# Kernel optimization log

Hardware: AMD Instinct MI355X
Metric: run time of the kernel (lower is better)

Reference implementation:

```python
import jax, jax.numpy as jnp
import numpy as np

D_MODEL = 1024
HEADS = 16
HEAD_DIM = D_MODEL // HEADS


def setup_inputs() -> dict:
    key = jax.random.key(0)
    k1, k2 = jax.random.split(key)
    x = jax.random.normal(k1, (2, 2048, D_MODEL), dtype=jnp.float32)
    # nn.Linear(d_model, 3*d_model, bias=False): weight shape [3*d_model, d_model]
    W_qkv = jax.random.normal(k2, (3 * D_MODEL, D_MODEL), dtype=jnp.float32) * (D_MODEL ** -0.5)
    return {"x": x, "W_qkv": W_qkv}


def reference(x, W_qkv):
    b, t, c = x.shape
    qkv = jnp.einsum('btc,fc->btf', x, W_qkv)  # [b, t, 3c]
    q, k, v = jnp.split(qkv, 3, axis=-1)
    # [b, heads, t, head_dim]
    q = q.reshape(b, t, HEADS, HEAD_DIM).transpose(0, 2, 1, 3)
    k = k.reshape(b, t, HEADS, HEAD_DIM).transpose(0, 2, 1, 3)
    v = v.reshape(b, t, HEADS, HEAD_DIM).transpose(0, 2, 1, 3)
    scores = jnp.einsum('bhqd,bhkd->bhqk', q, k) * (HEAD_DIM ** -0.5)
    causal = jnp.tril(jnp.ones((t, t), dtype=bool))  # [t, t]
    scores = jnp.where(causal[None, None, :, :], scores, -jnp.inf)
    weights = jax.nn.softmax(scores, axis=-1)
    out = jnp.einsum('bhqk,bhkd->bhqd', weights, v)
    return out.transpose(0, 2, 1, 3).reshape(b, t, c)
```

## Files before the change

kernel.cpp:

```cpp
#include <hip/hip_runtime.h>
#include <hip/hip_bf16.h>
#include <stdint.h>

#define D_MODEL 1024
#define TOKENS  2048
#define HEADS   16
#define HDIM    64
#define NQKV    3072
#define MROWS   4096
#define SCALE   0.18033688011112042f

typedef __attribute__((ext_vector_type(4)))  float f32x4;
typedef __attribute__((ext_vector_type(16))) float f32x16;
typedef __attribute__((ext_vector_type(8)))  short bf16x8;

__device__ __forceinline__ unsigned short f2bf(float f) {
  union { float f; unsigned u; } v; v.f = f;
  unsigned u = v.u + 0x7FFFu + ((v.u >> 16) & 1u);
  return (unsigned short)(u >> 16);
}
__device__ __forceinline__ float bf2f(unsigned short b) {
  union { unsigned u; float f; } v; v.u = ((unsigned)b) << 16;
  return v.f;
}
__device__ __forceinline__ unsigned cvt_pk_bf16(float lo, float hi) {
  unsigned r;
  asm("v_cvt_pk_bf16_f32 %0, %1, %2" : "=v"(r) : "v"(lo), "v"(hi));
  return r;
}
__device__ __forceinline__ float xchg32(float v) {
  return __shfl_xor(v, 32);
}
__device__ __forceinline__ bf16x8 pfrag8(const float* g) {
  union { uint4 u; bf16x8 v; } r;
  r.u.x = cvt_pk_bf16(g[0], g[1]);
  r.u.y = cvt_pk_bf16(g[2], g[3]);
  r.u.z = cvt_pk_bf16(g[4], g[5]);
  r.u.w = cvt_pk_bf16(g[6], g[7]);
  return r.v;
}
__device__ __forceinline__ float max32t(const f32x16& a, const f32x16& b) {
  float t[16];
#pragma unroll
  for (int r = 0; r < 16; ++r) t[r] = fmaxf(a[r], b[r]);
#pragma unroll
  for (int s = 8; s > 0; s >>= 1)
#pragma unroll
    for (int r = 0; r < s; ++r) t[r] = fmaxf(t[r], t[r + s]);
  return t[0];
}
__device__ __forceinline__ float sum32t(const float* a, const float* b) {
  float t[16];
#pragma unroll
  for (int r = 0; r < 16; ++r) t[r] = a[r] + b[r];
#pragma unroll
  for (int s = 8; s > 0; s >>= 1)
#pragma unroll
    for (int r = 0; r < s; ++r) t[r] = t[r] + t[r + s];
  return t[0];
}

#define GLOAD16(g, l)                                                          \
  __builtin_amdgcn_global_load_lds(                                            \
      (const __attribute__((address_space(1))) unsigned int*)(g),              \
      (__attribute__((address_space(3))) unsigned int*)(l), 16, 0, 0)

__global__ __launch_bounds__(256) void cvt_bf16(const float* __restrict__ X,
                                                const float* __restrict__ W,
                                                unsigned short* __restrict__ Xb,
                                                unsigned short* __restrict__ Wb) {
  const size_t NX = (size_t)MROWS * D_MODEL;
  size_t i = ((size_t)blockIdx.x * 256 + threadIdx.x) * 8;
  const float* src; unsigned short* dst; size_t off;
  if (i < NX) { src = X; dst = Xb; off = i; }
  else        { src = W; dst = Wb; off = i - NX; }
  float4 a = ((const float4*)(src + off))[0];
  float4 b = ((const float4*)(src + off))[1];
  union { unsigned short s[8]; uint4 v; } u;
  u.s[0] = f2bf(a.x); u.s[1] = f2bf(a.y); u.s[2] = f2bf(a.z); u.s[3] = f2bf(a.w);
  u.s[4] = f2bf(b.x); u.s[5] = f2bf(b.y); u.s[6] = f2bf(b.z); u.s[7] = f2bf(b.w);
  *(uint4*)(dst + off) = u.v;
}

__global__ __launch_bounds__(512, 1) void gemm8(const unsigned short* __restrict__ A,
                                                const unsigned short* __restrict__ B,
                                                unsigned short* __restrict__ C) {
  __shared__ unsigned short sA[2][2][128][64];
  __shared__ unsigned short sB[2][2][128][64];

  const int tid  = threadIdx.x;
  const int lane = tid & 63;
  const int wave = tid >> 6;
  const int wr   = wave >> 2;
  const int wc   = wave & 3;
  const int l15  = lane & 15;
  const int lg   = lane >> 4;

  const int bm = blockIdx.x;
  const int bn = blockIdx.y;

  f32x4 acc[8][4];
#pragma unroll
  for (int i = 0; i < 8; ++i)
#pragma unroll
    for (int j = 0; j < 4; ++j)
#pragma unroll
      for (int r = 0; r < 4; ++r) acc[i][j][r] = 0.f;

  const int srow = tid >> 3;
  const int scb  = (tid & 7) * 16;
  const int ssce = (scb ^ ((srow & 7) << 4)) >> 1;

  const unsigned short* Ag = A + (size_t)(bm * 256) * D_MODEL;
  const unsigned short* Bg = B + (size_t)(bn * 256) * D_MODEL;

#define STG_A(buf, hf, t)                                                      \
  { GLOAD16(Ag + (size_t)((hf) * 128 + srow) * D_MODEL + (t) * 64 + ssce,      \
            (char*)&sA[buf][hf][0][0] + srow * 128 + scb);                     \
    GLOAD16(Ag + (size_t)((hf) * 128 + 64 + srow) * D_MODEL + (t) * 64 + ssce, \
            (char*)&sA[buf][hf][0][0] + 8192 + srow * 128 + scb); }
#define STG_B(buf, hf, t)                                                      \
  { GLOAD16(Bg + (size_t)((hf) * 128 + srow) * D_MODEL + (t) * 64 + ssce,      \
            (char*)&sB[buf][hf][0][0] + srow * 128 + scb);                     \
    GLOAD16(Bg + (size_t)((hf) * 128 + 64 + srow) * D_MODEL + (t) * 64 + ssce, \
            (char*)&sB[buf][hf][0][0] + 8192 + srow * 128 + scb); }

  const char* aBse[2] = { (const char*)&sA[0][wr][0][0], (const char*)&sA[1][wr][0][0] };
  const char* bBse[2] = { (const char*)&sB[0][wc >> 1][0][0], (const char*)&sB[1][wc >> 1][0][0] };
  const int swzl = (l15 & 7) << 4;
  const int cbs0 = (lg * 16) ^ swzl;
  const int cbs1 = (64 + lg * 16) ^ swzl;
  const int arow = l15 * 128;
  const int brow = ((wc & 1) * 64 + l15) * 128;

  bf16x8 aF[4][2];

#define DO_PHASE(qm, qn, buf, LD_A, STAGE_STMT, DO_VM)                         \
  {                                                                            \
    if (LD_A) {                                                                \
      _Pragma("unroll")                                                        \
      for (int i = 0; i < 4; ++i) {                                            \
        aF[i][0] = *(const bf16x8*)(aBse[buf] + ((qm)*4 + i) * 2048 + arow + cbs0); \
        aF[i][1] = *(const bf16x8*)(aBse[buf] + ((qm)*4 + i) * 2048 + arow + cbs1); \
      }                                                                        \
    }                                                                          \
    bf16x8 b_[2][2];                                                           \
    _Pragma("unroll")                                                          \
    for (int n = 0; n < 2; ++n) {                                              \
      b_[n][0] = *(const bf16x8*)(bBse[buf] + ((qn)*2 + n) * 2048 + brow + cbs0); \
      b_[n][1] = *(const bf16x8*)(bBse[buf] + ((qn)*2 + n) * 2048 + brow + cbs1); \
    }                                                                          \
    STAGE_STMT;                                                                \
    if (DO_VM) asm volatile("s_waitcnt vmcnt(2)" ::: "memory");                \
    __builtin_amdgcn_s_barrier();                                              \
    asm volatile("s_waitcnt lgkmcnt(0)" ::: "memory");                         \
    __builtin_amdgcn_sched_barrier(0);                                         \
    __builtin_amdgcn_s_setprio(1);                                             \
    _Pragma("unroll")                                                          \
    for (int ks = 0; ks < 2; ++ks)                                             \
      _Pragma("unroll")                                                        \
      for (int i = 0; i < 4; ++i)                                              \
        _Pragma("unroll")                                                      \
        for (int n = 0; n < 2; ++n)                                            \
          acc[(qm)*4 + i][(qn)*2 + n] = __builtin_amdgcn_mfma_f32_16x16x32_bf16( \
              aF[i][ks], b_[n][ks], acc[(qm)*4 + i][(qn)*2 + n], 0, 0, 0);     \
    __builtin_amdgcn_s_setprio(0);                                             \
    __builtin_amdgcn_s_barrier();                                              \
  }

  STG_A(0, 0, 0);
  STG_B(0, 0, 0);
  STG_A(0, 1, 0);
  STG_B(0, 1, 0);
  STG_B(1, 0, 1);
  asm volatile("s_waitcnt vmcnt(2)" ::: "memory");
  __builtin_amdgcn_s_barrier();

#pragma unroll 1
  for (int j = 0; j < 8; ++j) {
    const int t1 = 2 * j + 1;
    const int t2 = 2 * j + 2;
    const int t3 = 2 * j + 3;
    DO_PHASE(0, 0, 0, 1, { STG_A(1, 0, t1); }, 0);
    DO_PHASE(0, 1, 0, 0, { STG_A(1, 1, t1); }, 0);
    DO_PHASE(1, 0, 0, 1, { STG_B(1, 1, t1); }, 0);
    DO_PHASE(1, 1, 0, 0, { if (t2 < 16) STG_B(0, 0, t2); }, 1);
    DO_PHASE(0, 0, 1, 1, { if (t2 < 16) STG_A(0, 0, t2); }, 0);
    DO_PHASE(0, 1, 1, 0, { if (t2 < 16) STG_A(0, 1, t2); }, 0);
    DO_PHASE(1, 0, 1, 1, { if (t2 < 16) STG_B(0, 1, t2); }, 0);
    DO_PHASE(1, 1, 1, 0, { if (t3 < 16) STG_B(1, 0, t3); }, 1);
  }

  const int orow0 = bm * 256 + wr * 128 + lg * 4;
  const int ocol0 = bn * 256 + wc * 64 + l15;
#pragma unroll
  for (int mi = 0; mi < 8; ++mi)
#pragma unroll
    for (int ni = 0; ni < 4; ++ni)
#pragma unroll
      for (int r = 0; r < 4; ++r)
        C[(size_t)(orow0 + mi * 16 + r) * NQKV + ocol0 + ni * 16] = f2bf(acc[mi][ni][r]);
#undef STG_A
#undef STG_B
#undef DO_PHASE
}

__global__ __launch_bounds__(256) void qkv_gemm(const float* __restrict__ X,
                                                const float* __restrict__ W,
                                                unsigned short* __restrict__ QKV) {
  __shared__ unsigned short sA[128 * 32];
  __shared__ unsigned short sB[128 * 32];
  const int tid  = threadIdx.x;
  const int lane = tid & 63;
  const int wave = tid >> 6;
  const int wr = wave >> 1, wc = wave & 1;
  const int row0 = blockIdx.x * 128;
  const int col0 = blockIdx.y * 128;

  f32x4 acc[4][4];
#pragma unroll
  for (int i = 0; i < 4; ++i)
#pragma unroll
    for (int j = 0; j < 4; ++j)
#pragma unroll
      for (int r = 0; r < 4; ++r) acc[i][j][r] = 0.f;

  const int srow = tid >> 1;
  const int scol = (tid & 1) * 16;
  union U16 { unsigned short s[8]; uint4 v; };

#pragma unroll 1
  for (int k0 = 0; k0 < D_MODEL; k0 += 32) {
    {
      const float* ga = X + (size_t)(row0 + srow) * D_MODEL + k0 + scol;
      const float* gb = W + (size_t)(col0 + srow) * D_MODEL + k0 + scol;
      float va[16], vb[16];
#pragma unroll
      for (int i = 0; i < 4; ++i) {
        float4 t = ((const float4*)ga)[i];
        va[4*i+0] = t.x; va[4*i+1] = t.y; va[4*i+2] = t.z; va[4*i+3] = t.w;
        float4 u = ((const float4*)gb)[i];
        vb[4*i+0] = u.x; vb[4*i+1] = u.y; vb[4*i+2] = u.z; vb[4*i+3] = u.w;
      }
      U16 ua0, ua1, ub0, ub1;
#pragma unroll
      for (int e = 0; e < 8; ++e) {
        ua0.s[e] = f2bf(va[e]);   ua1.s[e] = f2bf(va[8 + e]);
        ub0.s[e] = f2bf(vb[e]);   ub1.s[e] = f2bf(vb[8 + e]);
      }
      *(uint4*)&sA[srow * 32 + scol + 0] = ua0.v;
      *(uint4*)&sA[srow * 32 + scol + 8] = ua1.v;
      *(uint4*)&sB[srow * 32 + scol + 0] = ub0.v;
      *(uint4*)&sB[srow * 32 + scol + 8] = ub1.v;
    }
    __syncthreads();

    const int lrow = lane & 15;
    const int lk   = (lane >> 4) * 8;
    bf16x8 av[4], bv[4];
#pragma unroll
    for (int i = 0; i < 4; ++i)
      av[i] = *(const bf16x8*)&sA[(wr * 64 + i * 16 + lrow) * 32 + lk];
#pragma unroll
    for (int j = 0; j < 4; ++j)
      bv[j] = *(const bf16x8*)&sB[(wc * 64 + j * 16 + lrow) * 32 + lk];
#pragma unroll
    for (int i = 0; i < 4; ++i)
#pragma unroll
      for (int j = 0; j < 4; ++j)
        acc[i][j] = __builtin_amdgcn_mfma_f32_16x16x32_bf16(av[i], bv[j], acc[i][j], 0, 0, 0);
    __syncthreads();
  }

  const int orow = row0 + wr * 64 + (lane >> 4) * 4;
  const int ocol = col0 + wc * 64 + (lane & 15);
#pragma unroll
  for (int i = 0; i < 4; ++i)
#pragma unroll
    for (int j = 0; j < 4; ++j)
#pragma unroll
      for (int r = 0; r < 4; ++r)
        QKV[(size_t)(orow + i * 16 + r) * NQKV + ocol + j * 16] = f2bf(acc[i][j][r]);
}

__global__ __launch_bounds__(256, 2) void attn12(const unsigned short* __restrict__ QKV,
                                                 float* __restrict__ Out) {
  __shared__ unsigned short sK [2][2][64 * 64];
  __shared__ unsigned short sVt[2][2][64 * 64];

  const int tid  = threadIdx.x;
  const int lane = tid & 63;
  const int wave = tid >> 6;
  const int l31  = lane & 31;
  const int hi   = lane >> 5;

  const int x = blockIdx.x;
  int bh, u;
  if (x < 256) { bh = x & 31; u = x >> 5; }
  else         { const int x2 = x - 256; bh = x2 & 31; u = 15 - (x2 >> 5); }

  const int b = bh >> 4, h = bh & 15;
  const int q0w  = u * 128 + wave * 32;
  const int qcol = q0w + l31;

  const unsigned short* Qbase = QKV + (size_t)(b * TOKENS) * NQKV + h * HDIM;
  const unsigned short* Kbase = Qbase + D_MODEL;
  const unsigned short* Vbase = Kbase + D_MODEL;

  bf16x8 qf[4];
  {
    const unsigned short* qrow = Qbase + (size_t)qcol * NQKV + hi * 8;
    union { unsigned short us[8]; bf16x8 v; ushort4 q[2]; } t;
#pragma unroll
    for (int dk = 0; dk < 4; ++dk) {
      t.q[0] = ((const ushort4*)(qrow + dk * 16))[0];
      t.q[1] = ((const ushort4*)(qrow + dk * 16))[1];
#pragma unroll
      for (int e = 0; e < 8; ++e) t.us[e] = f2bf(bf2f(t.us[e]) * SCALE);
      qf[dk] = t.v;
    }
  }

  f32x16 o0a, o0b, o1a, o1b;
#pragma unroll
  for (int r = 0; r < 16; ++r) { o0a[r] = 0.f; o0b[r] = 0.f; o1a[r] = 0.f; o1b[r] = 0.f; }
  float m = -1e30f, ll = 0.f;

  const int vk0 = (tid & 15) * 4;
  const int vd0 = (tid >> 4) * 4;
  ushort4 va0, va1, va2, va3, vb0, vb1, vb2, vb3;

  const int lane16 = lane * 16;

#define KGLOAD(kt, buf, s)                                                     \
  {                                                                            \
    _Pragma("unroll")                                                          \
    for (int g = 0; g < 2; ++g) {                                              \
      const int base = g * 4096 + wave * 1024;                                 \
      const int d = base + lane16;                                             \
      const int row = d >> 7;                                                  \
      const int grow = (row & 51) | ((row & 4) << 1) | ((row & 8) >> 1);       \
      const int cb = (d & 127) ^ ((row & 7) << 4);                             \
      GLOAD16(Kbase + (size_t)((kt) * 64 + grow) * NQKV + (cb >> 1),           \
              (char*)&sK[buf][s][0] + base + lane16);                          \
    }                                                                          \
  }

#define VLOAD2(pp)                                                             \
  {                                                                            \
    const unsigned short* vsA = Vbase + (size_t)((2*(pp)) * 64 + vk0) * NQKV + vd0;   \
    va0 = *(const ushort4*)(vsA);                                              \
    va1 = *(const ushort4*)(vsA + NQKV);                                       \
    va2 = *(const ushort4*)(vsA + 2 * NQKV);                                   \
    va3 = *(const ushort4*)(vsA + 3 * NQKV);                                   \
    const unsigned short* vsB = Vbase + (size_t)((2*(pp)+1) * 64 + vk0) * NQKV + vd0; \
    vb0 = *(const ushort4*)(vsB);                                              \
    vb1 = *(const ushort4*)(vsB + NQKV);                                       \
    vb2 = *(const ushort4*)(vsB + 2 * NQKV);                                   \
    vb3 = *(const ushort4*)(vsB + 3 * NQKV);                                   \
  }

#define VWRITE1(buf, s, t0, t1, t2, t3)                                        \
  {                                                                            \
    ushort4 c0, c1, c2, c3;                                                    \
    c0.x = t0.x; c0.y = t1.x; c0.z = t2.x; c0.w = t3.x;                        \
    c1.x = t0.y; c1.y = t1.y; c1.z = t2.y; c1.w = t3.y;                        \
    c2.x = t0.z; c2.y = t1.z; c2.z = t2.z; c2.w = t3.z;                        \
    c3.x = t0.w; c3.y = t1.w; c3.z = t2.w; c3.w = t3.w;                        \
    char* dV = (char*)&sVt[buf][s][0];                                         \
    _Pragma("unroll")                                                          \
    for (int e = 0; e < 4; ++e) {                                              \
      const int dim = vd0 + e;                                                 \
      const int o2 = (dim * 128 + vk0 * 2) ^ ((dim & 7) << 4);                 \
      ushort4 cc = (e == 0) ? c0 : (e == 1) ? c1 : (e == 2) ? c2 : c3;         \
      *(ushort4*)(dV + o2) = cc;                                               \
    }                                                                          \
  }

#define QKT(cK, rowbase, st)                                                   \
  {                                                                            \
    _Pragma("unroll")                                                          \
    for (int dk = 0; dk < 4; ++dk) {                                           \
      const int row = (rowbase);                                               \
      bf16x8 kf = *(const bf16x8*)((cK) + ((row * 128 + hi * 16 + dk * 32) ^ ((row & 7) << 4))); \
      st = __builtin_amdgcn_mfma_f32_32x32x16_bf16(kf, qf[dk], st, 0, 0, 0);   \
    }                                                                          \
  }

#define PV4(cV, bpX, bpY, koff)                                                \
  {                                                                            \
    const int r0 = l31, r1 = l31 + 32;                                         \
    bf16x8 vf;                                                                 \
    vf = *(const bf16x8*)((cV) + ((r0 * 128 + hi * 16 + (koff)) ^ ((r0 & 7) << 4)));      \
    o0a = __builtin_amdgcn_mfma_f32_32x32x16_bf16(vf, bpX, o0a, 0, 0, 0);      \
    vf = *(const bf16x8*)((cV) + ((r1 * 128 + hi * 16 + (koff)) ^ ((r1 & 7) << 4)));      \
    o1a = __builtin_amdgcn_mfma_f32_32x32x16_bf16(vf, bpX, o1a, 0, 0, 0);      \
    vf = *(const bf16x8*)((cV) + ((r0 * 128 + hi * 16 + (koff) + 32) ^ ((r0 & 7) << 4))); \
    o0b = __builtin_amdgcn_mfma_f32_32x32x16_bf16(vf, bpY, o0b, 0, 0, 0);      \
    vf = *(const bf16x8*)((cV) + ((r1 * 128 + hi * 16 + (koff) + 32) ^ ((r1 & 7) << 4))); \
    o1b = __builtin_amdgcn_mfma_f32_32x32x16_bf16(vf, bpY, o1b, 0, 0, 0);      \
  }

#define MUPDATE(mx)                                                            \
  {                                                                            \
    if (!__all((mx) - m <= 8.f)) {                                             \
      float mw = fmaxf((mx), xchg32(mx));                                      \
      const float mnew = fmaxf(m, mw);                                         \
      const float corr = exp2f(m - mnew);                                      \
      m = mnew;                                                                \
      ll *= corr;                                                              \
      _Pragma("unroll")                                                        \
      for (int r = 0; r < 16; ++r) {                                           \
        o0a[r] *= corr; o0b[r] *= corr; o1a[r] *= corr; o1b[r] *= corr;        \
      }                                                                        \
    }                                                                          \
  }

  KGLOAD(0, 0, 0);
  KGLOAD(1, 0, 1);
  VLOAD2(0);
  VWRITE1(0, 0, va0, va1, va2, va3);
  VWRITE1(0, 1, vb0, vb1, vb2, vb3);
  __syncthreads();

#pragma unroll 1
  for (int p = 0; p < u; ++p) {
    const int cur = p & 1;
    KGLOAD(2 * (p + 1),     cur ^ 1, 0);
    KGLOAD(2 * (p + 1) + 1, cur ^ 1, 1);
    VLOAD2(p + 1);

    const char* cKA = (const char*)&sK[cur][0][0];
    const char* cKB = (const char*)&sK[cur][1][0];
    const char* cVA = (const char*)&sVt[cur][0][0];
    const char* cVB = (const char*)&sVt[cur][1][0];

    f32x16 sA0, sA1, sB0, sB1;
#pragma unroll
    for (int r = 0; r < 16; ++r) { sA0[r] = 0.f; sA1[r] = 0.f; sB0[r] = 0.f; sB1[r] = 0.f; }

    QKT(cKA, l31,      sA0);
    QKT(cKA, l31 + 32, sA1);
    QKT(cKB, l31,      sB0);
    QKT(cKB, l31 + 32, sB1);

    {
      float mx = max32t(sA0, sA1);
      MUPDATE(mx);
      float pA0[16], pA1[16];
#pragma unroll
      for (int r = 0; r < 16; ++r) { pA0[r] = exp2f(sA0[r] - m); pA1[r] = exp2f(sA1[r] - m); }
      ll += sum32t(pA0, pA1);
      bf16x8 a0 = pfrag8(&pA0[0]), a1 = pfrag8(&pA0[8]);
      bf16x8 a2 = pfrag8(&pA1[0]), a3 = pfrag8(&pA1[8]);
      PV4(cVA, a0, a1, 0);
      PV4(cVA, a2, a3, 64);
    }

    {
      float mx = max32t(sB0, sB1);
      MUPDATE(mx);
      float pB0[16], pB1[16];
#pragma unroll
      for (int r = 0; r < 16; ++r) { pB0[r] = exp2f(sB0[r] - m); pB1[r] = exp2f(sB1[r] - m); }
      ll += sum32t(pB0, pB1);
      bf16x8 b0 = pfrag8(&pB0[0]), b1 = pfrag8(&pB0[8]);
      bf16x8 b2 = pfrag8(&pB1[0]), b3 = pfrag8(&pB1[8]);
      PV4(cVB, b0, b1, 0);
      PV4(cVB, b2, b3, 64);
    }

    VWRITE1(cur ^ 1, 0, va0, va1, va2, va3);
    VWRITE1(cur ^ 1, 1, vb0, vb1, vb2, vb3);
    __syncthreads();
  }

  {
    const int cur = u & 1;
    const char* cK[2] = { (const char*)&sK[cur][0][0], (const char*)&sK[cur][1][0] };
    const char* cV[2] = { (const char*)&sVt[cur][0][0], (const char*)&sVt[cur][1][0] };
    const int nsub = (wave >= 2) ? 2 : 1;
#pragma unroll 1
    for (int s = 0; s < nsub; ++s) {
      const int kbase = u * 128 + s * 64;
      const bool diag  = (wave >= 2) ? (s == 1) : true;
      const bool do_hi = diag ? ((wave & 1) == 1) : true;

      f32x16 st0, st1;
#pragma unroll
      for (int r = 0; r < 16; ++r) { st0[r] = 0.f; st1[r] = 0.f; }

      QKT(cK[s], l31, st0);
      if (do_hi) QKT(cK[s], l31 + 32, st1);

      if (diag) {
#pragma unroll
        for (int r = 0; r < 16; ++r) {
          const int key0 = kbase + (r & 7) + ((r & 8) << 1) + 8 * hi;
          if (key0 > qcol) st0[r] = -1e30f;
          if (do_hi && key0 + 32 > qcol) st1[r] = -1e30f;
        }
      }

      float mx = do_hi ? max32t(st0, st1) : max32t(st0, st0);
      MUPDATE(mx);

      float p0[16], p1[16];
#pragma unroll
      for (int r = 0; r < 16; ++r) p0[r] = exp2f(st0[r] - m);
      if (do_hi) {
#pragma unroll
        for (int r = 0; r < 16; ++r) p1[r] = exp2f(st1[r] - m);
        ll += sum32t(p0, p1);
      } else {
        float z[16];
#pragma unroll
        for (int r = 0; r < 16; ++r) z[r] = 0.f;
        ll += sum32t(p0, z);
      }

      bf16x8 c0 = pfrag8(&p0[0]), c1 = pfrag8(&p0[8]);
      PV4(cV[s], c0, c1, 0);
      if (do_hi) {
        bf16x8 c2 = pfrag8(&p1[0]), c3 = pfrag8(&p1[8]);
        PV4(cV[s], c2, c3, 64);
      }
    }
  }

  {
    const float lfull = ll + xchg32(ll);
    const float inv = 1.f / lfull;
    float* orow = Out + (size_t)(b * TOKENS + qcol) * D_MODEL + h * HDIM;
#pragma unroll
    for (int g = 0; g < 4; ++g) {
      float4 w0, w1;
      w0.x = (o0a[4*g+0] + o0b[4*g+0]) * inv;
      w0.y = (o0a[4*g+1] + o0b[4*g+1]) * inv;
      w0.z = (o0a[4*g+2] + o0b[4*g+2]) * inv;
      w0.w = (o0a[4*g+3] + o0b[4*g+3]) * inv;
      w1.x = (o1a[4*g+0] + o1b[4*g+0]) * inv;
      w1.y = (o1a[4*g+1] + o1b[4*g+1]) * inv;
      w1.z = (o1a[4*g+2] + o1b[4*g+2]) * inv;
      w1.w = (o1a[4*g+3] + o1b[4*g+3]) * inv;
      *(float4*)(orow + 8 * g + 4 * hi)      = w0;
      *(float4*)(orow + 8 * g + 4 * hi + 32) = w1;
    }
  }
#undef KGLOAD
#undef VLOAD2
#undef VWRITE1
#undef QKT
#undef PV4
#undef MUPDATE
}

extern "C" void kernel_launch(void* const* d_in, const int* in_sizes, int n_in,
                              void* d_out, int out_size, void* d_ws, size_t ws_size,
                              hipStream_t stream) {
  const float* X = (const float*)d_in[0];
  const float* W = (const float*)d_in[1];
  float* Out = (float*)d_out;
  unsigned short* QKV = (unsigned short*)d_ws;

  const size_t QKV_E = (size_t)MROWS * NQKV;
  const size_t XB_E  = (size_t)MROWS * D_MODEL;
  const size_t WB_E  = (size_t)NQKV * D_MODEL;
  const size_t need_bf16 = (QKV_E + XB_E + WB_E) * 2;

  if (ws_size >= need_bf16) {
    unsigned short* Xb = QKV + QKV_E;
    unsigned short* Wb = Xb + XB_E;
    cvt_bf16<<<(XB_E + WB_E) / (256 * 8), 256, 0, stream>>>(X, W, Xb, Wb);
    gemm8<<<dim3(MROWS / 256, NQKV / 256), 512, 0, stream>>>(Xb, Wb, QKV);
  } else {
    qkv_gemm<<<dim3(MROWS / 128, NQKV / 128), 256, 0, stream>>>(X, W, QKV);
  }

  attn12<<<512, 256, 0, stream>>>(QKV, Out);
}
```

Baseline: 98.54 us.

## Split key blocks across two wave groups with split-softmax merge in attention

```diff
diff --git a/kernel.cpp b/kernel.cpp
--- a/kernel.cpp
+++ b/kernel.cpp
@@ -283,7 +283,7 @@
         QKV[(size_t)(orow + i * 16 + r) * NQKV + ocol + j * 16] = f2bf(acc[i][j][r]);
 }
 
-__global__ __launch_bounds__(256, 2) void attn12(const unsigned short* __restrict__ QKV,
+__global__ __launch_bounds__(512, 4) void attn13(const unsigned short* __restrict__ QKV,
                                                  float* __restrict__ Out) {
   __shared__ unsigned short sK [2][2][64 * 64];
   __shared__ unsigned short sVt[2][2][64 * 64];
@@ -291,6 +291,8 @@
   const int tid  = threadIdx.x;
   const int lane = tid & 63;
   const int wave = tid >> 6;
+  const int wq   = wave & 3;
+  const int ws   = wave >> 2;
   const int l31  = lane & 31;
   const int hi   = lane >> 5;
 
@@ -300,7 +302,7 @@
   else         { const int x2 = x - 256; bh = x2 & 31; u = 15 - (x2 >> 5); }
 
   const int b = bh >> 4, h = bh & 15;
-  const int q0w  = u * 128 + wave * 32;
+  const int q0w  = u * 128 + wq * 32;
   const int qcol = q0w + l31;
 
   const unsigned short* Qbase = QKV + (size_t)(b * TOKENS) * NQKV + h * HDIM;
@@ -326,54 +328,39 @@
   for (int r = 0; r < 16; ++r) { o0a[r] = 0.f; o0b[r] = 0.f; o1a[r] = 0.f; o1b[r] = 0.f; }
   float m = -1e30f, ll = 0.f;
 
-  const int vk0 = (tid & 15) * 4;
-  const int vd0 = (tid >> 4) * 4;
-  ushort4 va0, va1, va2, va3, vb0, vb1, vb2, vb3;
-
-  const int lane16 = lane * 16;
+  const int kd    = tid * 16;
+  const int krow  = kd >> 7;
+  const int kgrow = (krow & 51) | ((krow & 4) << 1) | ((krow & 8) >> 1);
+  const int kcb   = (kd & 127) ^ ((krow & 7) << 4);
+  const int vk0   = (tid & 31) * 2;
+  const int vd0   = (tid >> 5) * 4;
+  union VU { ushort4 v; unsigned short us[4]; };
+  VU va0, va1, vb0, vb1;
 
 #define KGLOAD(kt, buf, s)                                                     \
-  {                                                                            \
-    _Pragma("unroll")                                                          \
-    for (int g = 0; g < 2; ++g) {                                              \
-      const int base = g * 4096 + wave * 1024;                                 \
-      const int d = base + lane16;                                             \
-      const int row = d >> 7;                                                  \
-      const int grow = (row & 51) | ((row & 4) << 1) | ((row & 8) >> 1);       \
-      const int cb = (d & 127) ^ ((row & 7) << 4);                             \
-      GLOAD16(Kbase + (size_t)((kt) * 64 + grow) * NQKV + (cb >> 1),           \
-              (char*)&sK[buf][s][0] + base + lane16);                          \
-    }                                                                          \
-  }
-
-#define VLOAD2(pp)                                                             \
+  GLOAD16(Kbase + (size_t)((kt) * 64 + kgrow) * NQKV + (kcb >> 1),             \
+          (char*)&sK[buf][s][0] + kd);
+
+#define VLOADP(pp)                                                             \
   {                                                                            \
     const unsigned short* vsA = Vbase + (size_t)((2*(pp)) * 64 + vk0) * NQKV + vd0;   \
-    va0 = *(const ushort4*)(vsA);                                              \
-    va1 = *(const ushort4*)(vsA + NQKV);                                       \
-    va2 = *(const ushort4*)(vsA + 2 * NQKV);                                   \
-    va3 = *(const ushort4*)(vsA + 3 * NQKV);                                   \
+    va0.v = *(const ushort4*)(vsA);                                            \
+    va1.v = *(const ushort4*)(vsA + NQKV);                                     \
     const unsigned short* vsB = Vbase + (size_t)((2*(pp)+1) * 64 + vk0) * NQKV + vd0; \
-    vb0 = *(const ushort4*)(vsB);                                              \
-    vb1 = *(const ushort4*)(vsB + NQKV);                                       \
-    vb2 = *(const ushort4*)(vsB + 2 * NQKV);                                   \
-    vb3 = *(const ushort4*)(vsB + 3 * NQKV);                                   \
-  }
-
-#define VWRITE1(buf, s, t0, t1, t2, t3)                                        \
+    vb0.v = *(const ushort4*)(vsB);                                            \
+    vb1.v = *(const ushort4*)(vsB + NQKV);                                     \
+  }
+
+#define VWRITEP(buf)                                                           \
   {                                                                            \
-    ushort4 c0, c1, c2, c3;                                                    \
-    c0.x = t0.x; c0.y = t1.x; c0.z = t2.x; c0.w = t3.x;                        \
-    c1.x = t0.y; c1.y = t1.y; c1.z = t2.y; c1.w = t3.y;                        \
-    c2.x = t0.z; c2.y = t1.z; c2.z = t2.z; c2.w = t3.z;                        \
-    c3.x = t0.w; c3.y = t1.w; c3.z = t2.w; c3.w = t3.w;                        \
-    char* dV = (char*)&sVt[buf][s][0];                                         \
+    char* dA = (char*)&sVt[buf][0][0];                                         \
+    char* dB = (char*)&sVt[buf][1][0];                                         \
     _Pragma("unroll")                                                          \
     for (int e = 0; e < 4; ++e) {                                              \
       const int dim = vd0 + e;                                                 \
       const int o2 = (dim * 128 + vk0 * 2) ^ ((dim & 7) << 4);                 \
-      ushort4 cc = (e == 0) ? c0 : (e == 1) ? c1 : (e == 2) ? c2 : c3;         \
-      *(ushort4*)(dV + o2) = cc;                                               \
+      *(unsigned*)(dA + o2) = (unsigned)va0.us[e] | ((unsigned)va1.us[e] << 16); \
+      *(unsigned*)(dB + o2) = (unsigned)vb0.us[e] | ((unsigned)vb1.us[e] << 16); \
     }                                                                          \
   }
 
@@ -418,9 +405,8 @@
 
   KGLOAD(0, 0, 0);
   KGLOAD(1, 0, 1);
-  VLOAD2(0);
-  VWRITE1(0, 0, va0, va1, va2, va3);
-  VWRITE1(0, 1, vb0, vb1, vb2, vb3);
+  VLOADP(0);
+  VWRITEP(0);
   __syncthreads();
 
 #pragma unroll 1
@@ -428,70 +414,47 @@
     const int cur = p & 1;
     KGLOAD(2 * (p + 1),     cur ^ 1, 0);
     KGLOAD(2 * (p + 1) + 1, cur ^ 1, 1);
-    VLOAD2(p + 1);
-
-    const char* cKA = (const char*)&sK[cur][0][0];
-    const char* cKB = (const char*)&sK[cur][1][0];
-    const char* cVA = (const char*)&sVt[cur][0][0];
-    const char* cVB = (const char*)&sVt[cur][1][0];
-
-    f32x16 sA0, sA1, sB0, sB1;
-#pragma unroll
-    for (int r = 0; r < 16; ++r) { sA0[r] = 0.f; sA1[r] = 0.f; sB0[r] = 0.f; sB1[r] = 0.f; }
-
-    QKT(cKA, l31,      sA0);
-    QKT(cKA, l31 + 32, sA1);
-    QKT(cKB, l31,      sB0);
-    QKT(cKB, l31 + 32, sB1);
+    VLOADP(p + 1);
 
     {
-      float mx = max32t(sA0, sA1);
+      const char* cK = (const char*)&sK[cur][ws][0];
+      const char* cV = (const char*)&sVt[cur][ws][0];
+      f32x16 st0, st1;
+#pragma unroll
+      for (int r = 0; r < 16; ++r) { st0[r] = 0.f; st1[r] = 0.f; }
+      QKT(cK, l31,      st0);
+      QKT(cK, l31 + 32, st1);
+      float mx = max32t(st0, st1);
       MUPDATE(mx);
-      float pA0[16], pA1[16];
-#pragma unroll
-      for (int r = 0; r < 16; ++r) { pA0[r] = exp2f(sA0[r] - m); pA1[r] = exp2f(sA1[r] - m); }
-      ll += sum32t(pA0, pA1);
-      bf16x8 a0 = pfrag8(&pA0[0]), a1 = pfrag8(&pA0[8]);
-      bf16x8 a2 = pfrag8(&pA1[0]), a3 = pfrag8(&pA1[8]);
-      PV4(cVA, a0, a1, 0);
-      PV4(cVA, a2, a3, 64);
+      float p0[16], p1[16];
+#pragma unroll
+      for (int r = 0; r < 16; ++r) { p0[r] = exp2f(st0[r] - m); p1[r] = exp2f(st1[r] - m); }
+      ll += sum32t(p0, p1);
+      bf16x8 f0 = pfrag8(&p0[0]), f1 = pfrag8(&p0[8]);
+      bf16x8 f2 = pfrag8(&p1[0]), f3 = pfrag8(&p1[8]);
+      PV4(cV, f0, f1, 0);
+      PV4(cV, f2, f3, 64);
     }
 
-    {
-      float mx = max32t(sB0, sB1);
-      MUPDATE(mx);
-      float pB0[16], pB1[16];
-#pragma unroll
-      for (int r = 0; r < 16; ++r) { pB0[r] = exp2f(sB0[r] - m); pB1[r] = exp2f(sB1[r] - m); }
-      ll += sum32t(pB0, pB1);
-      bf16x8 b0 = pfrag8(&pB0[0]), b1 = pfrag8(&pB0[8]);
-      bf16x8 b2 = pfrag8(&pB1[0]), b3 = pfrag8(&pB1[8]);
-      PV4(cVB, b0, b1, 0);
-      PV4(cVB, b2, b3, 64);
-    }
-
-    VWRITE1(cur ^ 1, 0, va0, va1, va2, va3);
-    VWRITE1(cur ^ 1, 1, vb0, vb1, vb2, vb3);
+    VWRITEP(cur ^ 1);
     __syncthreads();
   }
 
   {
     const int cur = u & 1;
-    const char* cK[2] = { (const char*)&sK[cur][0][0], (const char*)&sK[cur][1][0] };
-    const char* cV[2] = { (const char*)&sVt[cur][0][0], (const char*)&sVt[cur][1][0] };
-    const int nsub = (wave >= 2) ? 2 : 1;
-#pragma unroll 1
-    for (int s = 0; s < nsub; ++s) {
-      const int kbase = u * 128 + s * 64;
-      const bool diag  = (wave >= 2) ? (s == 1) : true;
-      const bool do_hi = diag ? ((wave & 1) == 1) : true;
+    const bool skip = (ws == 1) && (wq < 2);
+    if (!skip) {
+      const bool diag  = (ws == 0) ? (wq < 2) : true;
+      const bool do_hi = diag ? ((wq & 1) == 1) : true;
+      const int kbase = u * 128 + ws * 64;
+      const char* cK = (const char*)&sK[cur][ws][0];
+      const char* cV = (const char*)&sVt[cur][ws][0];
 
       f32x16 st0, st1;
 #pragma unroll
       for (int r = 0; r < 16; ++r) { st0[r] = 0.f; st1[r] = 0.f; }
-
-      QKT(cK[s], l31, st0);
-      if (do_hi) QKT(cK[s], l31 + 32, st1);
+      QKT(cK, l31, st0);
+      if (do_hi) QKT(cK, l31 + 32, st1);
 
       if (diag) {
 #pragma unroll
@@ -520,36 +483,58 @@
       }
 
       bf16x8 c0 = pfrag8(&p0[0]), c1 = pfrag8(&p0[8]);
-      PV4(cV[s], c0, c1, 0);
+      PV4(cV, c0, c1, 0);
       if (do_hi) {
         bf16x8 c2 = pfrag8(&p1[0]), c3 = pfrag8(&p1[8]);
-        PV4(cV[s], c2, c3, 64);
+        PV4(cV, c2, c3, 64);
       }
     }
   }
 
-  {
-    const float lfull = ll + xchg32(ll);
-    const float inv = 1.f / lfull;
+  __syncthreads();
+  const float lfull = ll + xchg32(ll);
+#pragma unroll
+  for (int r = 0; r < 16; ++r) { o0a[r] += o0b[r]; o1a[r] += o1b[r]; }
+
+  float* slot = (wq < 2)
+      ? ((float*)&sK [0][0][0] + (size_t)(( wq      * 64 + lane) * 35))
+      : ((float*)&sVt[0][0][0] + (size_t)(((wq - 2) * 64 + lane) * 35));
+
+  if (ws == 1) {
+    slot[0] = m;
+    slot[1] = lfull;
+#pragma unroll
+    for (int r = 0; r < 16; ++r) slot[2 + r]  = o0a[r];
+#pragma unroll
+    for (int r = 0; r < 16; ++r) slot[18 + r] = o1a[r];
+  }
+  __syncthreads();
+  if (ws == 0) {
+    const float mB = slot[0];
+    const float lB = slot[1];
+    const float M  = fmaxf(m, mB);
+    const float wA = exp2f(m - M);
+    const float wB = exp2f(mB - M);
+    const float inv = 1.f / (lfull * wA + lB * wB);
     float* orow = Out + (size_t)(b * TOKENS + qcol) * D_MODEL + h * HDIM;
 #pragma unroll
     for (int g = 0; g < 4; ++g) {
       float4 w0, w1;
-      w0.x = (o0a[4*g+0] + o0b[4*g+0]) * inv;
-      w0.y = (o0a[4*g+1] + o0b[4*g+1]) * inv;
-      w0.z = (o0a[4*g+2] + o0b[4*g+2]) * inv;
-      w0.w = (o0a[4*g+3] + o0b[4*g+3]) * inv;
-      w1.x = (o1a[4*g+0] + o1b[4*g+0]) * inv;
-      w1.y = (o1a[4*g+1] + o1b[4*g+1]) * inv;
-      w1.z = (o1a[4*g+2] + o1b[4*g+2]) * inv;
-      w1.w = (o1a[4*g+3] + o1b[4*g+3]) * inv;
+      w0.x = (o0a[4*g+0] * wA + slot[2 + 4*g+0] * wB) * inv;
+      w0.y = (o0a[4*g+1] * wA + slot[2 + 4*g+1] * wB) * inv;
+      w0.z = (o0a[4*g+2] * wA + slot[2 + 4*g+2] * wB) * inv;
+      w0.w = (o0a[4*g+3] * wA + slot[2 + 4*g+3] * wB) * inv;
+      w1.x = (o1a[4*g+0] * wA + slot[18 + 4*g+0] * wB) * inv;
+      w1.y = (o1a[4*g+1] * wA + slot[18 + 4*g+1] * wB) * inv;
+      w1.z = (o1a[4*g+2] * wA + slot[18 + 4*g+2] * wB) * inv;
+      w1.w = (o1a[4*g+3] * wA + slot[18 + 4*g+3] * wB) * inv;
       *(float4*)(orow + 8 * g + 4 * hi)      = w0;
       *(float4*)(orow + 8 * g + 4 * hi + 32) = w1;
     }
   }
 #undef KGLOAD
-#undef VLOAD2
-#undef VWRITE1
+#undef VLOADP
+#undef VWRITEP
 #undef QKT
 #undef PV4
 #undef MUPDATE
@@ -577,5 +562,5 @@
     qkv_gemm<<<dim3(MROWS / 128, NQKV / 128), 256, 0, stream>>>(X, W, QKV);
   }
 
-  attn12<<<512, 256, 0, stream>>>(QKV, Out);
-}
+  attn13<<<512, 512, 0, stream>>>(QKV, Out);
+}
```

Measured after the change: 213.7 us. 117% more time.
